# Kernel optimization log

Measured on AMD Instinct MI355X. Metric: run time of the kernel, lower is better.

## Reference

```python
import jax, jax.numpy as jnp
import numpy as np

BATCH = 16384
INPUT_DIM = 1024
OUTPUT_DIM = 256
SCALES = 5  # pywt level = SCALES - 1

# pywt db4 decomposition low-pass filter (ascending index order)
DB4_LO = jnp.array([
    -0.010597401785069032, 0.0328830116668852, 0.030841381835560764,
    -0.18703481171909309, -0.027983769416859854, 0.6308807679298589,
    0.7148465705529157, 0.2303778133088965], dtype=jnp.float32)
# QMF: dec_hi[k] = (-1)^(k+1) * dec_lo[L-1-k]  (matches pywt sign convention)
_SIGNS = jnp.array([-1.0, 1.0, -1.0, 1.0, -1.0, 1.0, -1.0, 1.0], dtype=jnp.float32)
DB4_HI = DB4_LO[::-1] * _SIGNS


def _dwt_step(x, lo, hi):
    """Single-level pywt dwt with 'symmetric' mode along the last axis.
    x: [B, N] -> (cA, cD) each [B, floor((N+L-1)/2)]."""
    L = lo.shape[0]
    left = x[:, L - 2::-1]          # symmetric (half-point) left extension, L-1 samples
    right = x[:, -1:-L:-1]          # symmetric right extension, L-1 samples
    e = jnp.concatenate([left, x, right], axis=-1)[:, 1:]  # drop 1 to align odd-index downsample
    # convolution == correlation with reversed filter; stride-2 valid conv
    kern = jnp.stack([lo[::-1], hi[::-1]])[:, None, :]      # [2, 1, L]
    y = jax.lax.conv_general_dilated(
        e[:, None, :], kern, window_strides=(2,), padding='VALID',
        dimension_numbers=('NCW', 'OIW', 'NCW'))            # [B, 2, out_len]
    return y[:, 0], y[:, 1]


def _wavedec(x, level):
    """pywt.wavedec(x, 'db4', level) -> [cA_level, cD_level, ..., cD_1]."""
    ca = x
    details = []
    for _ in range(level):
        ca, cd = _dwt_step(ca, DB4_LO, DB4_HI)
        details.append(cd)
    return [ca] + details[::-1]


def setup_inputs() -> dict:
    key = jax.random.key(0)
    ks = jax.random.split(key, SCALES + 1)
    inp = {"x": jax.random.normal(ks[0], (BATCH, INPUT_DIM), dtype=jnp.float32)}
    for s in range(SCALES):
        inp[f"basis{s}"] = jax.random.normal(
            ks[s + 1], (INPUT_DIM // 2 ** s, OUTPUT_DIM), dtype=jnp.float32)
    return inp


def reference(x, basis0, basis1, basis2, basis3, basis4):
    bases = [basis0, basis1, basis2, basis3, basis4]
    coeffs = _wavedec(x, SCALES - 1)  # [cA4, cD4, cD3, cD2, cD1]
    out = jnp.zeros((x.shape[0], OUTPUT_DIM), dtype=x.dtype)
    for s in range(SCALES):
        m = min(coeffs[s].shape[-1], bases[s].shape[0])  # static; truncate to common length
        out = out + coeffs[s][:, :m] @ bases[s][:m]
    return out
```

## Files before the change

### kernel.cpp

```cpp
#include <hip/hip_runtime.h>

#define BATCH   16384
#define INDIM   1024
#define OUTDIM  256

constexpr int KP = 480;

__device__ __constant__ float LORc[8] = { 0.2303778133088965f,   0.7148465705529157f,
                                          0.6308807679298589f,  -0.027983769416859854f,
                                         -0.18703481171909309f,  0.030841381835560764f,
                                          0.0328830116668852f,  -0.010597401785069032f };
__device__ __constant__ float HIRc[8] = {-0.010597401785069032f, -0.0328830116668852f,
                                          0.030841381835560764f,  0.18703481171909309f,
                                         -0.027983769416859854f, -0.6308807679298589f,
                                          0.7148465705529157f,   -0.2303778133088965f };

__device__ __forceinline__ float symx(const float* __restrict__ in, int N, int t) {
    if (t < 0)  t = -1 - t;
    if (t >= N) t = 2 * N - 1 - t;
    return in[t];
}

__device__ __forceinline__ void dwt_level(const float* __restrict__ in, int N, int M,
                                          float* __restrict__ outA,
                                          float* __restrict__ outD, int nD, int lane) {
    for (int i = lane; i < M; i += 64) {
        const int base = 2 * i - 6;
        float a = 0.f, d = 0.f;
        if (base >= 0 && base + 7 < N) {
            #pragma unroll
            for (int k = 0; k < 8; ++k) {
                const float v = in[base + k];
                a = fmaf(v, LORc[k], a);
                d = fmaf(v, HIRc[k], d);
            }
        } else {
            #pragma unroll
            for (int k = 0; k < 8; ++k) {
                const float v = symx(in, N, base + k);
                a = fmaf(v, LORc[k], a);
                d = fmaf(v, HIRc[k], d);
            }
        }
        outA[i] = a;
        if (i < nD) outD[i] = d;
    }
}

extern "C" __global__ __launch_bounds__(256)
void dwt_ws(const float* __restrict__ x, float* __restrict__ coef)
{
    __shared__ float buf[4][1544];
    const int wid  = threadIdx.x >> 6;
    const int lane = threadIdx.x & 63;
    const int row  = blockIdx.x * 4 + wid;

    float* bufA = buf[wid];
    float* bufB = bufA + 1024;
    const float* xrow = x + (size_t)row * INDIM;
    float* crow = coef + (size_t)row * KP;

    #pragma unroll
    for (int j = 0; j < 4; ++j)
        ((float4*)bufA)[lane + 64 * j] = ((const float4*)xrow)[lane + 64 * j];
    __syncthreads();
    dwt_level(bufA, 1024, 515, bufB, crow + 408, 64, lane);
    __syncthreads();
    dwt_level(bufB, 515, 261, bufA, crow + 280, 128, lane);
    __syncthreads();
    dwt_level(bufA, 261, 134, bufB, crow + 144, 134, lane);
    __syncthreads();
    dwt_level(bufB, 134, 70, crow, crow + 72, 70, lane);
    if (lane < 14) {
        const int padidx[14] = {70,71,142,143,278,279,472,473,474,475,476,477,478,479};
        crow[padidx[lane]] = 0.f;
    }
}

extern "C" __global__ __launch_bounds__(256)
void pack_b(const float* __restrict__ b0, const float* __restrict__ b1,
            const float* __restrict__ b2, const float* __restrict__ b3,
            const float* __restrict__ b4, float* __restrict__ Bp)
{
    const int k = blockIdx.x;
    const int n = threadIdx.x;
    float v = 0.f;
    if      (k < 70)              v = b0[(size_t)k * OUTDIM + n];
    else if (k >= 72  && k < 142) v = b1[(size_t)(k - 72)  * OUTDIM + n];
    else if (k >= 144 && k < 278) v = b2[(size_t)(k - 144) * OUTDIM + n];
    else if (k >= 280 && k < 408) v = b3[(size_t)(k - 280) * OUTDIM + n];
    else if (k >= 408 && k < 472) v = b4[(size_t)(k - 408) * OUTDIM + n];
    Bp[(size_t)k * OUTDIM + n] = v;
}

extern "C" __global__ __launch_bounds__(256)
void gemm_f32(const float* __restrict__ A, const float* __restrict__ Bp,
              float* __restrict__ C)
{
    __shared__ float Al[2][16][68];
    __shared__ float Bl[2][16][128];

    const int tid = threadIdx.x;
    const int m0 = blockIdx.x * 64;
    const int n0 = blockIdx.y * 128;

    const int sa_m = tid >> 2;
    const int sa_k = (tid & 3) << 2;
    const int sb_k = tid >> 4;
    const int sb_n = (tid & 15) << 3;

    const float* Ap = A  + (size_t)(m0 + sa_m) * KP + sa_k;
    const float* Bq = Bp + (size_t)sb_k * OUTDIM + n0 + sb_n;

    const int rg = tid >> 4;
    const int cg = tid & 15;

    float acc[4][8];
    #pragma unroll
    for (int r = 0; r < 4; ++r)
        #pragma unroll
        for (int c = 0; c < 8; ++c) acc[r][c] = 0.f;

    float4 as, bs0, bs1;
    as  = *(const float4*)Ap;
    bs0 = *(const float4*)Bq;
    bs1 = *(const float4*)(Bq + 4);
    Al[0][sa_k + 0][sa_m] = as.x; Al[0][sa_k + 1][sa_m] = as.y;
    Al[0][sa_k + 2][sa_m] = as.z; Al[0][sa_k + 3][sa_m] = as.w;
    *(float4*)&Bl[0][sb_k][sb_n]     = bs0;
    *(float4*)&Bl[0][sb_k][sb_n + 4] = bs1;
    __syncthreads();

    int cur = 0;
    for (int t = 0; t < KP / 16; ++t) {
        if (t < KP / 16 - 1) {
            as  = *(const float4*)(Ap + (t + 1) * 16);
            bs0 = *(const float4*)(Bq + (size_t)(t + 1) * 16 * OUTDIM);
            bs1 = *(const float4*)(Bq + (size_t)(t + 1) * 16 * OUTDIM + 4);
        }
        #pragma unroll
        for (int k = 0; k < 16; ++k) {
            const float4 av  = *(const float4*)&Al[cur][k][rg << 2];
            const float4 bv0 = *(const float4*)&Bl[cur][k][cg << 3];
            const float4 bv1 = *(const float4*)&Bl[cur][k][(cg << 3) + 4];
            const float aa[4] = {av.x, av.y, av.z, av.w};
            const float bb[8] = {bv0.x, bv0.y, bv0.z, bv0.w, bv1.x, bv1.y, bv1.z, bv1.w};
            #pragma unroll
            for (int r = 0; r < 4; ++r)
                #pragma unroll
                for (int c = 0; c < 8; ++c)
                    acc[r][c] = fmaf(aa[r], bb[c], acc[r][c]);
        }
        if (t < KP / 16 - 1) {
            const int nx = cur ^ 1;
            Al[nx][sa_k + 0][sa_m] = as.x; Al[nx][sa_k + 1][sa_m] = as.y;
            Al[nx][sa_k + 2][sa_m] = as.z; Al[nx][sa_k + 3][sa_m] = as.w;
            *(float4*)&Bl[nx][sb_k][sb_n]     = bs0;
            *(float4*)&Bl[nx][sb_k][sb_n + 4] = bs1;
        }
        __syncthreads();
        cur ^= 1;
    }

    #pragma unroll
    for (int r = 0; r < 4; ++r) {
        float* cp = C + (size_t)(m0 + (rg << 2) + r) * OUTDIM + n0 + (cg << 3);
        *(float4*)cp       = float4{acc[r][0], acc[r][1], acc[r][2], acc[r][3]};
        *(float4*)(cp + 4) = float4{acc[r][4], acc[r][5], acc[r][6], acc[r][7]};
    }
}

constexpr int F_ROWS = 32;
constexpr int F_KP   = 472;

__device__ __forceinline__ void dwt_level_f(const float* __restrict__ in, int N, int M,
                                            float* __restrict__ outA,
                                            float* __restrict__ outD, int nD, int ht) {
    for (int i = ht; i < M; i += 128) {
        const int base = 2 * i - 6;
        float a = 0.f, d = 0.f;
        #pragma unroll
        for (int k = 0; k < 8; ++k) {
            const float v = symx(in, N, base + k);
            a = fmaf(v, LORc[k], a);
            d = fmaf(v, HIRc[k], d);
        }
        outA[i] = a;
        if (i < nD) outD[i] = d;
    }
}

extern "C" __global__ __launch_bounds__(256, 2)
void wkan_fused(const float* __restrict__ x,
                const float* __restrict__ b0, const float* __restrict__ b1,
                const float* __restrict__ b2, const float* __restrict__ b3,
                const float* __restrict__ b4,
                float* __restrict__ out)
{
    extern __shared__ float smem[];
    float* coef = smem;
    float* wbuf = smem + F_ROWS * F_KP;

    const int tid  = threadIdx.x;
    const int row0 = blockIdx.x * F_ROWS;

    for (int i = tid; i < F_ROWS * F_KP / 4; i += 256)
        ((float4*)coef)[i] = float4{0.f, 0.f, 0.f, 0.f};
    __syncthreads();

    const int slot = tid >> 7;
    const int ht   = tid & 127;
    float* bufA = wbuf + slot * 1544;
    float* bufB = bufA + 1024;

    for (int it = 0; it < F_ROWS / 2; ++it) {
        const int r = it * 2 + slot;
        float* crow = coef + r * F_KP;
        const float* xrow = x + (size_t)(row0 + r) * INDIM;
        ((float4*)bufA)[ht]       = ((const float4*)xrow)[ht];
        ((float4*)bufA)[ht + 128] = ((const float4*)xrow)[ht + 128];
        __syncthreads();
        dwt_level_f(bufA, 1024, 515, bufB, crow + 408, 64, ht);
        __syncthreads();
        dwt_level_f(bufB, 515, 261, bufA, crow + 280, 128, ht);
        __syncthreads();
        dwt_level_f(bufA, 261, 134, bufB, crow + 144, 134, ht);
        __syncthreads();
        dwt_level_f(bufB, 134, 70, crow, crow + 72, 70, ht);
        __syncthreads();
    }

    const int rg = tid >> 5;
    const int cg = tid & 31;
    float acc[4][8];
    #pragma unroll
    for (int r = 0; r < 4; ++r)
        #pragma unroll
        for (int c = 0; c < 8; ++c) acc[r][c] = 0.f;

    const float* Bs[5]  = { b0, b1, b2, b3, b4 };
    const int    off[5] = { 0, 72, 144, 280, 408 };
    const int    l4[5]  = { 72, 72, 136, 128, 64 };

    for (int s = 0; s < 5; ++s) {
        const float* __restrict__ B = Bs[s];
        const int o = off[s], L = l4[s];
        for (int k = 0; k < L; k += 4) {
            float4 bb[4][2];
            #pragma unroll
            for (int kk = 0; kk < 4; ++kk) {
                const float* bp = B + (size_t)(k + kk) * OUTDIM + cg * 8;
                bb[kk][0] = *(const float4*)(bp);
                bb[kk][1] = *(const float4*)(bp + 4);
            }
            #pragma unroll
            for (int rr = 0; rr < 4; ++rr) {
                const float4 c4 = *(const float4*)(coef + (rg * 4 + rr) * F_KP + o + k);
                const float cv[4] = { c4.x, c4.y, c4.z, c4.w };
                #pragma unroll
                for (int kk = 0; kk < 4; ++kk) {
                    acc[rr][0] = fmaf(cv[kk], bb[kk][0].x, acc[rr][0]);
                    acc[rr][1] = fmaf(cv[kk], bb[kk][0].y, acc[rr][1]);
                    acc[rr][2] = fmaf(cv[kk], bb[kk][0].z, acc[rr][2]);
                    acc[rr][3] = fmaf(cv[kk], bb[kk][0].w, acc[rr][3]);
                    acc[rr][4] = fmaf(cv[kk], bb[kk][1].x, acc[rr][4]);
                    acc[rr][5] = fmaf(cv[kk], bb[kk][1].y, acc[rr][5]);
                    acc[rr][6] = fmaf(cv[kk], bb[kk][1].z, acc[rr][6]);
                    acc[rr][7] = fmaf(cv[kk], bb[kk][1].w, acc[rr][7]);
                }
            }
        }
    }

    #pragma unroll
    for (int rr = 0; rr < 4; ++rr) {
        float* op = out + (size_t)(row0 + rg * 4 + rr) * OUTDIM + cg * 8;
        *(float4*)(op)     = float4{ acc[rr][0], acc[rr][1], acc[rr][2], acc[rr][3] };
        *(float4*)(op + 4) = float4{ acc[rr][4], acc[rr][5], acc[rr][6], acc[rr][7] };
    }
}

extern "C" void kernel_launch(void* const* d_in, const int* in_sizes, int n_in,
                              void* d_out, int out_size, void* d_ws, size_t ws_size,
                              hipStream_t stream) {
    const float* x  = (const float*)d_in[0];
    const float* b0 = (const float*)d_in[1];
    const float* b1 = (const float*)d_in[2];
    const float* b2 = (const float*)d_in[3];
    const float* b3 = (const float*)d_in[4];
    const float* b4 = (const float*)d_in[5];
    float* out = (float*)d_out;

    const size_t needA = (size_t)BATCH * KP * sizeof(float);
    const size_t needB = (size_t)KP * OUTDIM * sizeof(float);

    if (ws_size >= needA + needB) {
        float* wsA = (float*)d_ws;
        float* wsB = wsA + (size_t)BATCH * KP;
        hipLaunchKernelGGL(pack_b, dim3(KP), dim3(256), 0, stream,
                           b0, b1, b2, b3, b4, wsB);
        hipLaunchKernelGGL(dwt_ws, dim3(BATCH / 4), dim3(256), 0, stream, x, wsA);
        hipLaunchKernelGGL(gemm_f32, dim3(BATCH / 64, OUTDIM / 128), dim3(256), 0, stream,
                           wsA, wsB, out);
    } else {
        const size_t shmem = (size_t)(F_ROWS * F_KP + 2 * 1544) * sizeof(float);
        hipLaunchKernelGGL(wkan_fused, dim3(BATCH / F_ROWS), dim3(256), shmem, stream,
                           x, b0, b1, b2, b3, b4, out);
    }
}
```

Before: 176.0 us.

## Fold linear wavelet transform into weights and use split-bf16 MFMA GEMM

The DWT is linear, so the kernel now builds its 1024x480 matrix by transforming identity rows, multiplies that by the packed bases to get a 1024x256 effective weight, and then runs a single GEMM of x against it. The GEMM uses bf16 MFMA with a hi/lo split (three products) to stay close to fp32 accuracy. This removes the per-batch DWT pass and the coefficient workspace round trip, and replaces FP32 FMA with matrix cores. In exchange it adds small weight-preprocessing kernels on every call and a K of 1024 instead of 480, with some precision risk from dropping the lo*lo term.

```diff
diff --git a/kernel.cpp b/kernel.cpp
--- a/kernel.cpp
+++ b/kernel.cpp
@@ -1,10 +1,14 @@
 #include <hip/hip_runtime.h>
+#include <stdint.h>
 
 #define BATCH   16384
 #define INDIM   1024
 #define OUTDIM  256
 
 constexpr int KP = 480;
+
+typedef __attribute__((ext_vector_type(8))) short short8;
+typedef __attribute__((ext_vector_type(4))) float f32x4;
 
 __device__ __constant__ float LORc[8] = { 0.2303778133088965f,   0.7148465705529157f,
                                           0.6308807679298589f,  -0.027983769416859854f,
@@ -47,8 +51,18 @@
     }
 }
 
+__device__ __forceinline__ ushort f2bf_rne(float f) {
+    union { float f; uint32_t u; } v; v.f = f;
+    uint32_t r = v.u + 0x7fffu + ((v.u >> 16) & 1u);
+    return (ushort)(r >> 16);
+}
+__device__ __forceinline__ float bf2f(ushort h) {
+    union { uint32_t u; float f; } v; v.u = ((uint32_t)h) << 16;
+    return v.f;
+}
+
 extern "C" __global__ __launch_bounds__(256)
-void dwt_ws(const float* __restrict__ x, float* __restrict__ coef)
+void dwt_id(float* __restrict__ Wc)
 {
     __shared__ float buf[4][1544];
     const int wid  = threadIdx.x >> 6;
@@ -57,12 +71,9 @@
 
     float* bufA = buf[wid];
     float* bufB = bufA + 1024;
-    const float* xrow = x + (size_t)row * INDIM;
-    float* crow = coef + (size_t)row * KP;
-
-    #pragma unroll
-    for (int j = 0; j < 4; ++j)
-        ((float4*)bufA)[lane + 64 * j] = ((const float4*)xrow)[lane + 64 * j];
+    float* crow = Wc + (size_t)row * KP;
+
+    for (int j = lane; j < 1024; j += 64) bufA[j] = (j == row) ? 1.f : 0.f;
     __syncthreads();
     dwt_level(bufA, 1024, 515, bufB, crow + 408, 64, lane);
     __syncthreads();
@@ -94,80 +105,166 @@
 }
 
 extern "C" __global__ __launch_bounds__(256)
-void gemm_f32(const float* __restrict__ A, const float* __restrict__ Bp,
-              float* __restrict__ C)
-{
-    __shared__ float Al[2][16][68];
-    __shared__ float Bl[2][16][128];
-
+void wgemm(const float* __restrict__ Wc, const float* __restrict__ Bp,
+           float* __restrict__ W)
+{
+    __shared__ float wc[4][KP];
     const int tid = threadIdx.x;
-    const int m0 = blockIdx.x * 64;
-    const int n0 = blockIdx.y * 128;
-
-    const int sa_m = tid >> 2;
-    const int sa_k = (tid & 3) << 2;
-    const int sb_k = tid >> 4;
-    const int sb_n = (tid & 15) << 3;
-
-    const float* Ap = A  + (size_t)(m0 + sa_m) * KP + sa_k;
-    const float* Bq = Bp + (size_t)sb_k * OUTDIM + n0 + sb_n;
-
-    const int rg = tid >> 4;
-    const int cg = tid & 15;
-
-    float acc[4][8];
+    const int r0  = blockIdx.x * 4;
+
     #pragma unroll
     for (int r = 0; r < 4; ++r)
-        #pragma unroll
-        for (int c = 0; c < 8; ++c) acc[r][c] = 0.f;
-
-    float4 as, bs0, bs1;
-    as  = *(const float4*)Ap;
-    bs0 = *(const float4*)Bq;
-    bs1 = *(const float4*)(Bq + 4);
-    Al[0][sa_k + 0][sa_m] = as.x; Al[0][sa_k + 1][sa_m] = as.y;
-    Al[0][sa_k + 2][sa_m] = as.z; Al[0][sa_k + 3][sa_m] = as.w;
-    *(float4*)&Bl[0][sb_k][sb_n]     = bs0;
-    *(float4*)&Bl[0][sb_k][sb_n + 4] = bs1;
-    __syncthreads();
-
-    int cur = 0;
-    for (int t = 0; t < KP / 16; ++t) {
-        if (t < KP / 16 - 1) {
-            as  = *(const float4*)(Ap + (t + 1) * 16);
-            bs0 = *(const float4*)(Bq + (size_t)(t + 1) * 16 * OUTDIM);
-            bs1 = *(const float4*)(Bq + (size_t)(t + 1) * 16 * OUTDIM + 4);
-        }
-        #pragma unroll
-        for (int k = 0; k < 16; ++k) {
-            const float4 av  = *(const float4*)&Al[cur][k][rg << 2];
-            const float4 bv0 = *(const float4*)&Bl[cur][k][cg << 3];
-            const float4 bv1 = *(const float4*)&Bl[cur][k][(cg << 3) + 4];
-            const float aa[4] = {av.x, av.y, av.z, av.w};
-            const float bb[8] = {bv0.x, bv0.y, bv0.z, bv0.w, bv1.x, bv1.y, bv1.z, bv1.w};
+        for (int k = tid; k < KP; k += 256)
+            wc[r][k] = Wc[(size_t)(r0 + r) * KP + k];
+    __syncthreads();
+
+    float acc[4] = {0.f, 0.f, 0.f, 0.f};
+    for (int k = 0; k < KP; ++k) {
+        const float b = Bp[(size_t)k * OUTDIM + tid];
+        #pragma unroll
+        for (int r = 0; r < 4; ++r) acc[r] = fmaf(wc[r][k], b, acc[r]);
+    }
+    #pragma unroll
+    for (int r = 0; r < 4; ++r) W[(size_t)(r0 + r) * OUTDIM + tid] = acc[r];
+}
+
+extern "C" __global__ __launch_bounds__(256)
+void bpack(const float* __restrict__ W, ushort* __restrict__ Bpk)
+{
+    const int slot  = blockIdx.x * 256 + threadIdx.x;
+    const int chunk = slot >> 10;
+    const int nf    = (slot >> 6) & 15;
+    const int lane  = slot & 63;
+    const int k     = chunk * 32 + (lane >> 4) * 8;
+    const int n     = nf * 16 + (lane & 15);
+
+    ushort hi[8], lo[8];
+    #pragma unroll
+    for (int j = 0; j < 8; ++j) {
+        const float w = W[(size_t)(k + j) * OUTDIM + n];
+        hi[j] = f2bf_rne(w);
+        lo[j] = f2bf_rne(w - bf2f(hi[j]));
+    }
+    const size_t base = ((size_t)(chunk * 16 + nf) * 2) * 64 * 8 + (size_t)lane * 8;
+    #pragma unroll
+    for (int j = 0; j < 8; ++j) {
+        Bpk[base + j]           = hi[j];
+        Bpk[base + 512 + j]     = lo[j];
+    }
+}
+
+extern "C" __global__ __launch_bounds__(512)
+void wkan_mfma(const float* __restrict__ x, const ushort* __restrict__ Bpk,
+               float* __restrict__ out)
+{
+    __shared__ ushort Ah[2][2][2][64][8];
+    __shared__ ushort Bb[16][2][64][8];
+
+    const int tid  = threadIdx.x;
+    const int lane = tid & 63;
+    const int wid  = tid >> 6;
+    const int wm   = wid >> 2;
+    const int wn   = wid & 3;
+    const int row0 = blockIdx.x * 64;
+
+    f32x4 acc[2][4];
+    #pragma unroll
+    for (int m = 0; m < 2; ++m)
+        #pragma unroll
+        for (int f = 0; f < 4; ++f) acc[m][f] = f32x4{0.f, 0.f, 0.f, 0.f};
+
+    const int s_wm   = tid >> 7;
+    const int s_mf   = (tid >> 6) & 1;
+    const int s_lane = tid & 63;
+    const int s_row  = s_wm * 32 + s_mf * 16 + (s_lane & 15);
+    const int s_kg   = s_lane >> 4;
+    const float* xrow = x + (size_t)(row0 + s_row) * INDIM + s_kg * 8;
+
+    float4 af0, af1;
+    uint4  bs0, bs1, bs2, bs3;
+
+    {
+        const ushort* bp = Bpk + (size_t)tid * 8;
+        bs0 = *(const uint4*)(bp);
+        bs1 = *(const uint4*)(bp + 4096);
+        bs2 = *(const uint4*)(bp + 8192);
+        bs3 = *(const uint4*)(bp + 12288);
+        if (tid < 256) {
+            af0 = *(const float4*)(xrow);
+            af1 = *(const float4*)(xrow + 4);
+        }
+    }
+
+    for (int c = 0; c < 32; ++c) {
+        {
+            ushort* bbf = &Bb[0][0][0][0] + (size_t)tid * 8;
+            *(uint4*)(bbf)         = bs0;
+            *(uint4*)(bbf + 4096)  = bs1;
+            *(uint4*)(bbf + 8192)  = bs2;
+            *(uint4*)(bbf + 12288) = bs3;
+        }
+        if (tid < 256) {
+            const float a[8] = {af0.x, af0.y, af0.z, af0.w, af1.x, af1.y, af1.z, af1.w};
+            uint32_t hw[4], lw[4];
+            #pragma unroll
+            for (int p = 0; p < 4; ++p) {
+                const ushort h0 = f2bf_rne(a[2*p]),   h1 = f2bf_rne(a[2*p+1]);
+                const ushort l0 = f2bf_rne(a[2*p]   - bf2f(h0));
+                const ushort l1 = f2bf_rne(a[2*p+1] - bf2f(h1));
+                hw[p] = (uint32_t)h0 | ((uint32_t)h1 << 16);
+                lw[p] = (uint32_t)l0 | ((uint32_t)l1 << 16);
+            }
+            *(uint4*)&Ah[0][s_wm][s_mf][s_lane][0] = uint4{hw[0], hw[1], hw[2], hw[3]};
+            *(uint4*)&Ah[1][s_wm][s_mf][s_lane][0] = uint4{lw[0], lw[1], lw[2], lw[3]};
+        }
+        __syncthreads();
+
+        if (c < 31) {
+            const ushort* bp = Bpk + (size_t)(c + 1) * 16384 + (size_t)tid * 8;
+            bs0 = *(const uint4*)(bp);
+            bs1 = *(const uint4*)(bp + 4096);
+            bs2 = *(const uint4*)(bp + 8192);
+            bs3 = *(const uint4*)(bp + 12288);
+            if (tid < 256) {
+                af0 = *(const float4*)(xrow + (c + 1) * 32);
+                af1 = *(const float4*)(xrow + (c + 1) * 32 + 4);
+            }
+        }
+
+        short8 afr[2][2];
+        #pragma unroll
+        for (int h = 0; h < 2; ++h)
+            #pragma unroll
+            for (int m = 0; m < 2; ++m)
+                afr[h][m] = *(const short8*)&Ah[h][wm][m][lane][0];
+        short8 bfr[4][2];
+        #pragma unroll
+        for (int f = 0; f < 4; ++f)
+            #pragma unroll
+            for (int h = 0; h < 2; ++h)
+                bfr[f][h] = *(const short8*)&Bb[wn * 4 + f][h][lane][0];
+
+        #pragma unroll
+        for (int m = 0; m < 2; ++m)
+            #pragma unroll
+            for (int f = 0; f < 4; ++f) {
+                acc[m][f] = __builtin_amdgcn_mfma_f32_16x16x32_bf16(afr[0][m], bfr[f][0], acc[m][f], 0, 0, 0);
+                acc[m][f] = __builtin_amdgcn_mfma_f32_16x16x32_bf16(afr[0][m], bfr[f][1], acc[m][f], 0, 0, 0);
+                acc[m][f] = __builtin_amdgcn_mfma_f32_16x16x32_bf16(afr[1][m], bfr[f][0], acc[m][f], 0, 0, 0);
+            }
+        __syncthreads();
+    }
+
+    #pragma unroll
+    for (int m = 0; m < 2; ++m)
+        #pragma unroll
+        for (int f = 0; f < 4; ++f) {
+            const int col = wn * 64 + f * 16 + (lane & 15);
+            const int rowb = row0 + wm * 32 + m * 16 + (lane >> 4) * 4;
             #pragma unroll
             for (int r = 0; r < 4; ++r)
-                #pragma unroll
-                for (int c = 0; c < 8; ++c)
-                    acc[r][c] = fmaf(aa[r], bb[c], acc[r][c]);
-        }
-        if (t < KP / 16 - 1) {
-            const int nx = cur ^ 1;
-            Al[nx][sa_k + 0][sa_m] = as.x; Al[nx][sa_k + 1][sa_m] = as.y;
-            Al[nx][sa_k + 2][sa_m] = as.z; Al[nx][sa_k + 3][sa_m] = as.w;
-            *(float4*)&Bl[nx][sb_k][sb_n]     = bs0;
-            *(float4*)&Bl[nx][sb_k][sb_n + 4] = bs1;
-        }
-        __syncthreads();
-        cur ^= 1;
-    }
-
-    #pragma unroll
-    for (int r = 0; r < 4; ++r) {
-        float* cp = C + (size_t)(m0 + (rg << 2) + r) * OUTDIM + n0 + (cg << 3);
-        *(float4*)cp       = float4{acc[r][0], acc[r][1], acc[r][2], acc[r][3]};
-        *(float4*)(cp + 4) = float4{acc[r][4], acc[r][5], acc[r][6], acc[r][7]};
-    }
+                out[(size_t)(rowb + r) * OUTDIM + col] = acc[m][f][r];
+        }
 }
 
 constexpr int F_ROWS = 32;
@@ -291,17 +388,23 @@
     const float* b4 = (const float*)d_in[5];
     float* out = (float*)d_out;
 
-    const size_t needA = (size_t)BATCH * KP * sizeof(float);
-    const size_t needB = (size_t)KP * OUTDIM * sizeof(float);
-
-    if (ws_size >= needA + needB) {
-        float* wsA = (float*)d_ws;
-        float* wsB = wsA + (size_t)BATCH * KP;
-        hipLaunchKernelGGL(pack_b, dim3(KP), dim3(256), 0, stream,
-                           b0, b1, b2, b3, b4, wsB);
-        hipLaunchKernelGGL(dwt_ws, dim3(BATCH / 4), dim3(256), 0, stream, x, wsA);
-        hipLaunchKernelGGL(gemm_f32, dim3(BATCH / 64, OUTDIM / 128), dim3(256), 0, stream,
-                           wsA, wsB, out);
+    const size_t nWc  = (size_t)1024 * KP;
+    const size_t nBp  = (size_t)KP * OUTDIM;
+    const size_t nW   = (size_t)1024 * OUTDIM;
+    const size_t nBpk = (size_t)1024 * OUTDIM * 2;
+    const size_t need = (nWc + nBp + nW) * 4 + nBpk * 2;
+
+    if (ws_size >= need) {
+        float*  Wc  = (float*)d_ws;
+        float*  Bp  = Wc + nWc;
+        float*  W   = Bp + nBp;
+        ushort* Bpk = (ushort*)(W + nW);
+
+        hipLaunchKernelGGL(pack_b,  dim3(KP),   dim3(256), 0, stream, b0, b1, b2, b3, b4, Bp);
+        hipLaunchKernelGGL(dwt_id,  dim3(256),  dim3(256), 0, stream, Wc);
+        hipLaunchKernelGGL(wgemm,   dim3(256),  dim3(256), 0, stream, Wc, Bp, W);
+        hipLaunchKernelGGL(bpack,   dim3(128),  dim3(256), 0, stream, W, Bpk);
+        hipLaunchKernelGGL(wkan_mfma, dim3(BATCH / 64), dim3(512), 0, stream, x, Bpk, out);
     } else {
         const size_t shmem = (size_t)(F_ROWS * F_KP + 2 * 1544) * sizeof(float);
         hipLaunchKernelGGL(wkan_fused, dim3(BATCH / F_ROWS), dim3(256), shmem, stream,
```

Result: no change. 175.9 us (-0.1%).
